# Kernel optimization log

Measured on AMD Instinct MI355X. Metric: run time of the kernel, lower is better.

The kernel has to match this reference:

```python
import jax, jax.numpy as jnp
import numpy as np


def setup_inputs() -> dict:
    key = jax.random.key(0)
    k1, k2, k3 = jax.random.split(key, 3)
    B, T, C, SIDE = 64, 12, 64, 32
    S2 = SIDE * SIDE
    d = jax.random.normal(k1, (B, T, C, S2), dtype=jnp.float32)
    m = jax.random.randint(k2, (B, T, C, S2), 0, 2, dtype=jnp.int32)
    # zero out even-indexed cells at the last time step so that roughly half the
    # cells trigger the "all-observations-missing" branch (the POI gather path)
    cell_keep = (jnp.arange(S2) % 2).astype(jnp.int32)  # [S2]
    m = m.at[:, -1].set(m[:, -1] * cell_keep[None, None, :])
    poi_index = jax.random.randint(k3, (S2,), 0, S2, dtype=jnp.int64)
    return {"d": d, "m": m, "poi_index": poi_index, "side": SIDE}


def reference(d, m, poi_index, side):
    B, T, C, S2 = d.shape
    data = d[:, -1].reshape(B, C, S2)          # [B, C, side*side]
    mask = m[:, -1].reshape(B, C, S2)          # [B, C, side*side]
    # original loop: for each cell i, if mask[:, :, i].sum() == 0 then
    # poicmp[:, :, i] = data[:, :, poi_index[i]] else 0 -- vectorized:
    cell_empty = (mask.sum(axis=(0, 1)) == 0)  # [S2] bool predicate per cell
    gathered = data[:, :, poi_index]            # [B, C, S2] neighbor gather
    poicmp = jnp.where(cell_empty[None, None, :], gathered, jnp.float32(0))
    data_poi = (data + poicmp).reshape(B, C, side, side)
    return data_poi
```

## Files before the change

### kernel.cpp

```cpp
#include <hip/hip_runtime.h>

#define B_  64
#define T_  12
#define C_  64
#define S2_ 1024

__global__ void mask_reduce(const int* __restrict__ m, int* __restrict__ flags) {
    const int cc = blockIdx.x & 3;
    const int b  = blockIdx.x >> 2;
    const int s  = cc * 256 + threadIdx.x;
    const int* row = m + ((size_t)(b * T_ + (T_ - 1)) * C_) * S2_ + s;
    int acc = 0;
#pragma unroll
    for (int c = 0; c < C_; ++c) acc |= row[(size_t)c * S2_];
    if (acc) atomicOr(&flags[s], 1);
}

__global__ void auxcmp_main(const float* __restrict__ d,
                            const int* __restrict__ flags,
                            const int* __restrict__ poi,
                            float* __restrict__ out) {
    const int i  = (blockIdx.x * 256 + threadIdx.x) * 4;
    const int bc = i >> 10;
    const int s  = i & (S2_ - 1);
    const int b  = bc >> 6;
    const int c  = bc & 63;
    const size_t dbase = ((size_t)(b * T_ + (T_ - 1)) * C_ + c) * S2_;

    const float4 v = *(const float4*)(d + dbase + s);
    const int4  f  = *(const int4*)(flags + s);
    const int4  p  = *(const int4*)(poi + s);

    float4 o = v;
    if (f.x == 0) o.x += d[dbase + p.x];
    if (f.y == 0) o.y += d[dbase + p.y];
    if (f.z == 0) o.z += d[dbase + p.z];
    if (f.w == 0) o.w += d[dbase + p.w];

    *(float4*)(out + i) = o;
}

extern "C" void kernel_launch(void* const* d_in, const int* in_sizes, int n_in,
                              void* d_out, int out_size, void* d_ws, size_t ws_size,
                              hipStream_t stream) {
    const float* d   = (const float*)d_in[0];
    const int*   m   = (const int*)d_in[1];
    const int*   poi = (const int*)d_in[2];
    float*       out = (float*)d_out;
    int*         flags = (int*)d_ws;

    hipMemsetAsync(flags, 0, S2_ * sizeof(int), stream);

    mask_reduce<<<dim3(256), dim3(256), 0, stream>>>(m, flags);

    auxcmp_main<<<dim3((B_ * C_ * S2_) / (256 * 4)), dim3(256), 0, stream>>>(
        d, flags, poi, out);
}
```

Measured before the change: 316.0 us.

## Replace atomic mask reduction with partial buffers and per-block final reduce

The memset and atomicOr-based flag reduction are replaced by a kernel that writes per-(batch, channel-half) partial OR results with int4 loads. The main kernel then ORs all 128 partials into shared memory in every block and processes 16 rows per block over 256 blocks instead of one float4 per thread over 4096 blocks. This removes the memset launch and the atomics. In exchange, every block redundantly reads a 512KB partial buffer, and the main kernel runs as a much smaller grid.

```diff
diff --git a/kernel.cpp b/kernel.cpp
--- a/kernel.cpp
+++ b/kernel.cpp
@@ -5,39 +5,57 @@
 #define C_  64
 #define S2_ 1024
 
-__global__ void mask_reduce(const int* __restrict__ m, int* __restrict__ flags) {
-    const int cc = blockIdx.x & 3;
-    const int b  = blockIdx.x >> 2;
-    const int s  = cc * 256 + threadIdx.x;
-    const int* row = m + ((size_t)(b * T_ + (T_ - 1)) * C_) * S2_ + s;
-    int acc = 0;
+__global__ void mask_partial(const int* __restrict__ m, int* __restrict__ partial) {
+    const int ch = blockIdx.x & 1;
+    const int b  = blockIdx.x >> 1;
+    const int s4 = threadIdx.x * 4;
+    const int* base = m + ((size_t)(b * T_ + (T_ - 1)) * C_ + ch * 32) * S2_;
+    int4 acc = make_int4(0, 0, 0, 0);
 #pragma unroll
-    for (int c = 0; c < C_; ++c) acc |= row[(size_t)c * S2_];
-    if (acc) atomicOr(&flags[s], 1);
+    for (int c = 0; c < 32; ++c) {
+        const int4 v = *(const int4*)(base + (size_t)c * S2_ + s4);
+        acc.x |= v.x; acc.y |= v.y; acc.z |= v.z; acc.w |= v.w;
+    }
+    *(int4*)(partial + (size_t)blockIdx.x * S2_ + s4) = acc;
 }
 
-__global__ void auxcmp_main(const float* __restrict__ d,
-                            const int* __restrict__ flags,
-                            const int* __restrict__ poi,
-                            float* __restrict__ out) {
-    const int i  = (blockIdx.x * 256 + threadIdx.x) * 4;
-    const int bc = i >> 10;
-    const int s  = i & (S2_ - 1);
-    const int b  = bc >> 6;
-    const int c  = bc & 63;
-    const size_t dbase = ((size_t)(b * T_ + (T_ - 1)) * C_ + c) * S2_;
+__global__ void auxcmp(const float* __restrict__ d,
+                       const int* __restrict__ partial,
+                       const int* __restrict__ poi,
+                       float* __restrict__ out) {
+    __shared__ int sflags[S2_];
+    const int t  = threadIdx.x;
+    const int s4 = t * 4;
 
-    const float4 v = *(const float4*)(d + dbase + s);
-    const int4  f  = *(const int4*)(flags + s);
-    const int4  p  = *(const int4*)(poi + s);
+    int4 f = make_int4(0, 0, 0, 0);
+#pragma unroll 8
+    for (int p = 0; p < 128; ++p) {
+        const int4 v = *(const int4*)(partial + (size_t)p * S2_ + s4);
+        f.x |= v.x; f.y |= v.y; f.z |= v.z; f.w |= v.w;
+    }
+    *(int4*)(sflags + s4) = f;
+    __syncthreads();
 
-    float4 o = v;
-    if (f.x == 0) o.x += d[dbase + p.x];
-    if (f.y == 0) o.y += d[dbase + p.y];
-    if (f.z == 0) o.z += d[dbase + p.z];
-    if (f.w == 0) o.w += d[dbase + p.w];
+    const int4 fl = *(const int4*)(sflags + s4);
+    const int4 p4 = *(const int4*)(poi + s4);
 
-    *(float4*)(out + i) = o;
+    const int row0 = blockIdx.x * 16;
+#pragma unroll
+    for (int i = 0; i < 16; ++i) {
+        const int row = row0 + i;
+        const int b = row >> 6;
+        const int c = row & 63;
+        const size_t dbase = ((size_t)(b * T_ + (T_ - 1)) * C_ + c) * S2_;
+
+        const float4 v = *(const float4*)(d + dbase + s4);
+        float4 o = v;
+        if (fl.x == 0) o.x += d[dbase + p4.x];
+        if (fl.y == 0) o.y += d[dbase + p4.y];
+        if (fl.z == 0) o.z += d[dbase + p4.z];
+        if (fl.w == 0) o.w += d[dbase + p4.w];
+
+        *(float4*)(out + (size_t)row * S2_ + s4) = o;
+    }
 }
 
 extern "C" void kernel_launch(void* const* d_in, const int* in_sizes, int n_in,
@@ -47,12 +65,8 @@
     const int*   m   = (const int*)d_in[1];
     const int*   poi = (const int*)d_in[2];
     float*       out = (float*)d_out;
-    int*         flags = (int*)d_ws;
+    int*         partial = (int*)d_ws;
 
-    hipMemsetAsync(flags, 0, S2_ * sizeof(int), stream);
-
-    mask_reduce<<<dim3(256), dim3(256), 0, stream>>>(m, flags);
-
-    auxcmp_main<<<dim3((B_ * C_ * S2_) / (256 * 4)), dim3(256), 0, stream>>>(
-        d, flags, poi, out);
+    mask_partial<<<dim3(128), dim3(256), 0, stream>>>(m, partial);
+    auxcmp<<<dim3(256), dim3(256), 0, stream>>>(d, partial, poi, out);
 }
```

New measurement: 328.5 us. 1.04x slower.
